# Kernel optimization log

Measured on AMD Instinct MI355X. Metric: run time of the kernel, lower is better.

## Reference

```python
import jax, jax.numpy as jnp
import numpy as np

# dims: L layers, D d_model, H heads, DH head_dim, DFF ffn, V vocab, BLK nf4 blocksize
L, D, H, DH, DFF, V, BLK = 2, 2048, 16, 128, 5504, 32000, 64
B, S, C, T = 4, 1000, 7, 45

# bitsandbytes NF4 codebook (fixed 16 quantiles of N(0,1), normalized to [-1,1])
NF4 = jnp.array([-1.0, -0.6961928009986877, -0.5250730514526367, -0.39491748809814453,
                 -0.28444138169288635, -0.18477343022823334, -0.09105003625154495, 0.0,
                 0.07958029955625534, 0.16093020141124725, 0.24611230194568634,
                 0.3379152417182922, 0.44070982933044434, 0.5626170039176941,
                 0.7229568362236023, 1.0], dtype=jnp.float32)


def _dequant(idx, scale):
    # idx: [out, in] int in [0,16); scale: [out, in//BLK] per-block absmax
    o, i = idx.shape
    return (NF4[idx].reshape(o, i // BLK, BLK) * scale[:, :, None]).reshape(o, i)


def _rmsnorm(h, w, eps=1e-5):
    return h * jax.lax.rsqrt(jnp.mean(h * h, axis=-1, keepdims=True) + eps) * w


def _rot_half(x):
    x1, x2 = jnp.split(x, 2, axis=-1)
    return jnp.concatenate([-x2, x1], axis=-1)


def _llama_fwd(token_ids, embed, wq_idx, wq_scale, wk_idx, wk_scale, wv_idx, wv_scale,
               wo_idx, wo_scale, wg_idx, wg_scale, wu_idx, wu_scale, wd_idx, wd_scale,
               ln1_w, ln2_w, lnf_w):
    Bt, St = token_ids.shape
    h = embed[token_ids]  # [B,S,D]
    # rotary embeddings
    inv = 1.0 / (10000.0 ** (jnp.arange(0, DH, 2, dtype=jnp.float32) / DH))
    ang = jnp.arange(St, dtype=jnp.float32)[:, None] * inv[None, :]  # [S, DH/2]
    emb_ang = jnp.concatenate([ang, ang], axis=-1)  # [S, DH]
    cos, sin = jnp.cos(emb_ang), jnp.sin(emb_ang)
    mask = jnp.where(jnp.tril(jnp.ones((St, St), dtype=bool)), 0.0, -1e9)  # causal
    for l in range(L):
        xn = _rmsnorm(h, ln1_w[l])
        q = (xn @ _dequant(wq_idx[l], wq_scale[l]).T).reshape(Bt, St, H, DH).transpose(0, 2, 1, 3)
        k = (xn @ _dequant(wk_idx[l], wk_scale[l]).T).reshape(Bt, St, H, DH).transpose(0, 2, 1, 3)
        v = (xn @ _dequant(wv_idx[l], wv_scale[l]).T).reshape(Bt, St, H, DH).transpose(0, 2, 1, 3)
        q = q * cos + _rot_half(q) * sin
        k = k * cos + _rot_half(k) * sin
        att = jax.nn.softmax(jnp.einsum('bhqd,bhkd->bhqk', q, k) / np.float32(np.sqrt(DH)) + mask, axis=-1)
        ctx = jnp.einsum('bhqk,bhkd->bhqd', att, v).transpose(0, 2, 1, 3).reshape(Bt, St, D)
        h = h + ctx @ _dequant(wo_idx[l], wo_scale[l]).T
        xn = _rmsnorm(h, ln2_w[l])
        g = xn @ _dequant(wg_idx[l], wg_scale[l]).T
        u = xn @ _dequant(wu_idx[l], wu_scale[l]).T
        h = h + (jax.nn.silu(g) * u) @ _dequant(wd_idx[l], wd_scale[l]).T
    # hidden_states[-1].mean(dim=1)
    return _rmsnorm(h, lnf_w).mean(axis=1)


def setup_inputs() -> dict:
    key = jax.random.key(0)
    ks = jax.random.split(key, 20)
    ridx = lambda k, shp: jax.random.randint(k, shp, 0, 16, dtype=jnp.int32)
    rsc = lambda k, shp: jax.random.uniform(k, shp, minval=0.01, maxval=0.03, dtype=jnp.float32)
    return {
        'x': jax.random.normal(ks[0], (B, C, T), dtype=jnp.float32),
        'token_ids': jax.random.randint(ks[1], (B, S), 0, V, dtype=jnp.int32),
        'embed': jax.random.normal(ks[2], (V, D), dtype=jnp.float32) * 0.02,
        'wq_idx': ridx(ks[3], (L, D, D)), 'wq_scale': rsc(ks[4], (L, D, D // BLK)),
        'wk_idx': ridx(ks[5], (L, D, D)), 'wk_scale': rsc(ks[6], (L, D, D // BLK)),
        'wv_idx': ridx(ks[7], (L, D, D)), 'wv_scale': rsc(ks[8], (L, D, D // BLK)),
        'wo_idx': ridx(ks[9], (L, D, D)), 'wo_scale': rsc(ks[10], (L, D, D // BLK)),
        'wg_idx': ridx(ks[11], (L, DFF, D)), 'wg_scale': rsc(ks[12], (L, DFF, D // BLK)),
        'wu_idx': ridx(ks[13], (L, DFF, D)), 'wu_scale': rsc(ks[14], (L, DFF, D // BLK)),
        'wd_idx': ridx(ks[15], (L, D, DFF)), 'wd_scale': rsc(ks[16], (L, D, DFF // BLK)),
        'ln1_w': jnp.ones((L, D), dtype=jnp.float32),
        'ln2_w': jnp.ones((L, D), dtype=jnp.float32),
        'lnf_w': jnp.ones((D,), dtype=jnp.float32),
        'proj_w': jax.random.normal(ks[17], (D, T), dtype=jnp.float32) * 0.05,
        'proj_b': jnp.zeros((D,), dtype=jnp.float32),
    }


def reference(x, token_ids, embed, wq_idx, wq_scale, wk_idx, wk_scale, wv_idx, wv_scale,
              wo_idx, wo_scale, wg_idx, wg_scale, wu_idx, wu_scale, wd_idx, wd_scale,
              ln1_w, ln2_w, lnf_w, proj_w, proj_b):
    # NF4-quantized Llama-style causal LM forward + mean pool over sequence
    e_text = _llama_fwd(token_ids, embed, wq_idx, wq_scale, wk_idx, wk_scale, wv_idx, wv_scale,
                        wo_idx, wo_scale, wg_idx, wg_scale, wu_idx, wu_scale, wd_idx, wd_scale,
                        ln1_w, ln2_w, lnf_w)  # [B, D]
    # series branch: channel-mean -> linear -> L2 normalize
    series_mean = x.mean(axis=1)  # [B, T]
    series_emb = series_mean @ proj_w.T + proj_b  # [B, D]
    series_emb = series_emb / jnp.maximum(jnp.linalg.norm(series_emb, axis=-1, keepdims=True), 1e-12)
    return e_text + series_emb
```

## Files before the change

kernel.cpp:

```cpp
#include <hip/hip_runtime.h>
#include <hip/hip_bf16.h>

#define L_N 2
#define D_ 2048
#define H_ 16
#define DH_ 128
#define DFF_ 5504
#define B_ 4
#define S_ 1000
#define C_ 7
#define T_ 45
#define M_ 4000

typedef short bf16x8 __attribute__((ext_vector_type(8)));
typedef float f32x4 __attribute__((ext_vector_type(4)));

__constant__ float NF4_TAB[16] = {
  -1.0f, -0.6961928009986877f, -0.5250730514526367f, -0.39491748809814453f,
  -0.28444138169288635f, -0.18477343022823334f, -0.09105003625154495f, 0.0f,
  0.07958029955625534f, 0.16093020141124725f, 0.24611230194568634f,
  0.3379152417182922f, 0.44070982933044434f, 0.5626170039176941f,
  0.7229568362236023f, 1.0f };

__device__ __forceinline__ unsigned short f2bf(float f) {
  unsigned int u = __float_as_uint(f);
  u += 0x7fffu + ((u >> 16) & 1u);
  return (unsigned short)(u >> 16);
}
__device__ __forceinline__ float bf2f(unsigned short u) {
  return __uint_as_float(((unsigned int)u) << 16);
}
__device__ __forceinline__ f32x4 zero4() { f32x4 z; z[0]=0.f; z[1]=0.f; z[2]=0.f; z[3]=0.f; return z; }
__device__ __forceinline__ f32x4 mfma16(bf16x8 a, bf16x8 b, f32x4 c) {
  return __builtin_amdgcn_mfma_f32_16x16x32_bf16(a, b, c, 0, 0, 0);
}

typedef __attribute__((address_space(3))) unsigned int lds_u32;
typedef const __attribute__((address_space(1))) unsigned int glb_u32;
__device__ __forceinline__ void gload16(const void* g, void* l) {
  __builtin_amdgcn_global_load_lds((glb_u32*)g, (lds_u32*)l, 16, 0, 0);
}

__global__ void rope_tables(float* __restrict__ cosT, float* __restrict__ sinT) {
  int s = blockIdx.x, d = threadIdx.x;
  int j = d & 63;
  float inv = expf(-(float)j * (9.210340371976184f / 64.f));
  float ang = (float)s * inv;
  cosT[s * DH_ + d] = cosf(ang);
  sinT[s * DH_ + d] = sinf(ang);
}

__global__ __launch_bounds__(256) void embed_gather(const int* __restrict__ tok,
    const float* __restrict__ emb, float* __restrict__ h) {
  int row = blockIdx.x;
  int tk = tok[row];
  const float4* src = reinterpret_cast<const float4*>(emb + (size_t)tk * D_);
  float4* dst = reinterpret_cast<float4*>(h + (size_t)row * D_);
  dst[threadIdx.x] = src[threadIdx.x];
  dst[threadIdx.x + 256] = src[threadIdx.x + 256];
}

__global__ __launch_bounds__(256) void rmsnorm_k(float* __restrict__ h,
    const float* __restrict__ add, const float* __restrict__ w,
    unsigned short* __restrict__ out) {
  const int row = blockIdx.x, t = threadIdx.x;
  float* hp = h + (size_t)row * D_;
  float4 a = *reinterpret_cast<const float4*>(&hp[t * 8]);
  float4 b = *reinterpret_cast<const float4*>(&hp[t * 8 + 4]);
  if (add) {
    const float* ap = add + (size_t)row * D_;
    float4 da = *reinterpret_cast<const float4*>(&ap[t * 8]);
    float4 db = *reinterpret_cast<const float4*>(&ap[t * 8 + 4]);
    a.x += da.x; a.y += da.y; a.z += da.z; a.w += da.w;
    b.x += db.x; b.y += db.y; b.z += db.z; b.w += db.w;
    *reinterpret_cast<float4*>(&hp[t * 8]) = a;
    *reinterpret_cast<float4*>(&hp[t * 8 + 4]) = b;
  }
  float ss = a.x*a.x + a.y*a.y + a.z*a.z + a.w*a.w
           + b.x*b.x + b.y*b.y + b.z*b.z + b.w*b.w;
#pragma unroll
  for (int m = 1; m < 64; m <<= 1) ss += __shfl_xor(ss, m);
  __shared__ float red[4];
  if ((t & 63) == 0) red[t >> 6] = ss;
  __syncthreads();
  float tot = red[0] + red[1] + red[2] + red[3];
  float rs = rsqrtf(tot * (1.0f / D_) + 1e-5f);
  float4 wa = *reinterpret_cast<const float4*>(&w[t * 8]);
  float4 wb = *reinterpret_cast<const float4*>(&w[t * 8 + 4]);
  unsigned r0 = (unsigned)f2bf(a.x*rs*wa.x) | ((unsigned)f2bf(a.y*rs*wa.y) << 16);
  unsigned r1 = (unsigned)f2bf(a.z*rs*wa.z) | ((unsigned)f2bf(a.w*rs*wa.w) << 16);
  unsigned r2 = (unsigned)f2bf(b.x*rs*wb.x) | ((unsigned)f2bf(b.y*rs*wb.y) << 16);
  unsigned r3 = (unsigned)f2bf(b.z*rs*wb.z) | ((unsigned)f2bf(b.w*rs*wb.w) << 16);
  int4 ov; ov.x = (int)r0; ov.y = (int)r1; ov.z = (int)r2; ov.w = (int)r3;
  *reinterpret_cast<int4*>(&out[(size_t)row * D_ + t * 8]) = ov;
}

struct DqJob { const int* idx; const float* sc; unsigned short* out; };
struct DqBatch { DqJob j[4]; };

__global__ __launch_bounds__(256) void dequant_batch(DqBatch bt, int K) {
  __shared__ float nf4[16];
  const int t = threadIdx.x;
  if (t < 16) nf4[t] = NF4_TAB[t];
  __syncthreads();
  const DqJob jb = bt.j[blockIdx.z];
  const int row = blockIdx.y;
  const int k0 = blockIdx.x * 2048 + t * 8;
  if (k0 >= K) return;
  const size_t base = (size_t)row * K + k0;
  int4 a = *reinterpret_cast<const int4*>(&jb.idx[base]);
  int4 b = *reinterpret_cast<const int4*>(&jb.idx[base + 4]);
  float s = jb.sc[(size_t)row * (K >> 6) + (k0 >> 6)];
  unsigned r0 = (unsigned)f2bf(nf4[a.x & 15] * s) | ((unsigned)f2bf(nf4[a.y & 15] * s) << 16);
  unsigned r1 = (unsigned)f2bf(nf4[a.z & 15] * s) | ((unsigned)f2bf(nf4[a.w & 15] * s) << 16);
  unsigned r2 = (unsigned)f2bf(nf4[b.x & 15] * s) | ((unsigned)f2bf(nf4[b.y & 15] * s) << 16);
  unsigned r3 = (unsigned)f2bf(nf4[b.z & 15] * s) | ((unsigned)f2bf(nf4[b.w & 15] * s) << 16);
  int4 ov; ov.x = (int)r0; ov.y = (int)r1; ov.z = (int)r2; ov.w = (int)r3;
  *reinterpret_cast<int4*>(&jb.out[base]) = ov;
}

template<int MODE>
__global__ __launch_bounds__(256, 4) void gemm_pipe(
    const unsigned short* __restrict__ A,
    const unsigned short* __restrict__ Bw,
    const unsigned short* __restrict__ Bw2,
    int Mdim, int N, int K,
    void* outp, void* outp2) {
  __shared__ unsigned short A_lds[2][128 * 64];
  __shared__ unsigned short B_lds[2][128 * 64];
  const int t = threadIdx.x;
  const int lane = t & 63, wid = t >> 6;
  const int z = blockIdx.z;

  const unsigned short* Bsrc = (MODE == 0 && z) ? Bw2 : Bw;
  void* osel = (MODE == 0 && z) ? outp2 : outp;

  const int bid = blockIdx.x;
  const int xcd = bid & 7, l = bid >> 3;
  const int m_blk = xcd * 4 + (l & 3);
  const int n_blk = l >> 2;
  const int n0 = n_blk * 128;
  const int m0 = m_blk * 128;

  const int wm = (wid >> 1) * 64, wn = (wid & 1) * 64;
  const int lr = lane & 15, lg = lane >> 4;
  const int lrow = lane >> 3;
  const int lslot = (((lane & 7) ^ lrow) << 4);
  const int rswz = (lr & 7) << 4;

  f32x4 acc[4][4];
#pragma unroll
  for (int i = 0; i < 4; ++i)
#pragma unroll
    for (int j = 0; j < 4; ++j) acc[i][j] = zero4();

  const int kT = K >> 6;
  const size_t rowb = (size_t)(K * 2);

  auto stage = [&](int kt, int b) {
#pragma unroll
    for (int c0 = 0; c0 < 4; ++c0) {
      const int c = wid + 4 * c0;
      int gr = m0 + c * 8 + lrow;
      gr = gr < Mdim ? gr : Mdim - 1;
      gload16((const char*)A + (size_t)gr * rowb + kt * 128 + lslot,
              (char*)&A_lds[b][0] + c * 1024);
      const int nr = n0 + c * 8 + lrow;
      gload16((const char*)Bsrc + (size_t)nr * rowb + kt * 128 + lslot,
              (char*)&B_lds[b][0] + c * 1024);
    }
  };

  stage(0, 0);
  for (int kt = 0; kt < kT; ++kt) {
    const int cur = kt & 1;
    if (kt + 1 < kT) {
      stage(kt + 1, cur ^ 1);
      asm volatile("s_waitcnt vmcnt(8)" ::: "memory");
    } else {
      asm volatile("s_waitcnt vmcnt(0)" ::: "memory");
    }
    __builtin_amdgcn_s_barrier();
    __builtin_amdgcn_sched_barrier(0);
#pragma unroll
    for (int ks = 0; ks < 2; ++ks) {
      bf16x8 af[4], bfr[4];
      const int cb = (ks * 64 + lg * 16) ^ rswz;
#pragma unroll
      for (int i = 0; i < 4; ++i) {
        af[i]  = *reinterpret_cast<const bf16x8*>(
                   (const char*)&A_lds[cur][0] + (wm + i * 16 + lr) * 128 + cb);
        bfr[i] = *reinterpret_cast<const bf16x8*>(
                   (const char*)&B_lds[cur][0] + (wn + i * 16 + lr) * 128 + cb);
      }
      __builtin_amdgcn_s_setprio(1);
#pragma unroll
      for (int mi = 0; mi < 4; ++mi)
#pragma unroll
        for (int ni = 0; ni < 4; ++ni)
          acc[mi][ni] = mfma16(af[mi], bfr[ni], acc[mi][ni]);
      __builtin_amdgcn_s_setprio(0);
    }
    __builtin_amdgcn_s_barrier();
  }

#pragma unroll
  for (int mi = 0; mi < 4; ++mi) {
#pragma unroll
    for (int r = 0; r < 4; ++r) {
      int gm = m0 + wm + mi * 16 + lg * 4 + r;
      if (gm >= Mdim) continue;
#pragma unroll
      for (int ni = 0; ni < 4; ++ni) {
        int gn = n0 + wn + ni * 16 + lr;
        float v = acc[mi][ni][r];
        if (MODE == 0) {
          ((unsigned short*)osel)[(size_t)gm * N + gn] = f2bf(v);
        } else {
          const int which = gn >> 11;
          const int hh = (gn >> 7) & 15, dd = gn & 127;
          const int b = gm / S_, s = gm - b * S_;
          ((unsigned short*)outp)[
            (((size_t)which * (B_ * H_) + b * H_ + hh) * S_ + s) * DH_ + dd] = f2bf(v);
        }
      }
    }
  }
}

template<int MODE>
__global__ __launch_bounds__(256, 4) void gemm_bf16(
    const unsigned short* __restrict__ A,
    const unsigned short* __restrict__ Bw,
    const unsigned short* __restrict__ Bw2,
    int Mdim, int N, int K, int nx, int ksplit,
    void* outp, void* outp2, float* dscr) {
  __shared__ unsigned short A_lds[128 * 64];
  __shared__ unsigned short B_lds[128 * 64];
  const int t = threadIdx.x;
  const int lane = t & 63, wid = t >> 6;
  const int z = blockIdx.z;

  const unsigned short* Bsrc = (MODE == 0 && z) ? Bw2 : Bw;
  void* osel = (MODE == 0 && z) ? outp2 : outp;

  const int bid = blockIdx.x;
  const int xcd = bid & 7, l = bid >> 3;
  const int m_blk = xcd * 4 + (l & 3);
  const int n_blk = l >> 2;
  const int n0 = n_blk * 128;
  const int m0 = m_blk * 128;

  const int wm = (wid >> 1) * 64, wn = (wid & 1) * 64;
  const int lr = lane & 15, lg = lane >> 4;
  const int lrow = lane >> 3;
  const int lslot = (((lane & 7) ^ lrow) << 4);
  const int rswz = (lr & 7) << 4;

  f32x4 acc[4][4];
#pragma unroll
  for (int i = 0; i < 4; ++i)
#pragma unroll
    for (int j = 0; j < 4; ++j) acc[i][j] = zero4();

  const int kT = K >> 6;
  const int ktlo = (MODE == 3) ? (z ? ksplit : 0) : 0;
  const int kthi = (MODE == 3) ? (z ? kT : ksplit) : kT;
  const size_t rowb = (size_t)(K * 2);

  for (int kt = ktlo; kt < kthi; ++kt) {
#pragma unroll
    for (int c0 = 0; c0 < 4; ++c0) {
      const int c = wid + 4 * c0;
      int gr = m0 + c * 8 + lrow;
      gr = gr < Mdim ? gr : Mdim - 1;
      gload16((const char*)A + (size_t)gr * rowb + kt * 128 + lslot,
              (char*)&A_lds[0] + c * 1024);
      const int nr = n0 + c * 8 + lrow;
      gload16((const char*)Bsrc + (size_t)nr * rowb + kt * 128 + lslot,
              (char*)&B_lds[0] + c * 1024);
    }
    __syncthreads();
#pragma unroll
    for (int ks = 0; ks < 2; ++ks) {
      bf16x8 af[4], bfr[4];
      const int cb = (ks * 64 + lg * 16) ^ rswz;
#pragma unroll
      for (int i = 0; i < 4; ++i) {
        af[i]  = *reinterpret_cast<const bf16x8*>(
                   (const char*)&A_lds[0] + (wm + i * 16 + lr) * 128 + cb);
        bfr[i] = *reinterpret_cast<const bf16x8*>(
                   (const char*)&B_lds[0] + (wn + i * 16 + lr) * 128 + cb);
      }
      __builtin_amdgcn_s_setprio(1);
#pragma unroll
      for (int mi = 0; mi < 4; ++mi)
#pragma unroll
        for (int ni = 0; ni < 4; ++ni)
          acc[mi][ni] = mfma16(af[mi], bfr[ni], acc[mi][ni]);
      __builtin_amdgcn_s_setprio(0);
    }
    __syncthreads();
  }

#pragma unroll
  for (int mi = 0; mi < 4; ++mi) {
#pragma unroll
    for (int r = 0; r < 4; ++r) {
      int gm = m0 + wm + mi * 16 + lg * 4 + r;
      if (gm >= Mdim) continue;
#pragma unroll
      for (int ni = 0; ni < 4; ++ni) {
        int gn = n0 + wn + ni * 16 + lr;
        float v = acc[mi][ni][r];
        if (MODE == 0) {
          ((unsigned short*)osel)[(size_t)gm * N + gn] = f2bf(v);
        } else if (MODE == 1) {
          const int which = gn >> 11;
          const int hh = (gn >> 7) & 15, dd = gn & 127;
          const int b = gm / S_, s = gm - b * S_;
          ((unsigned short*)outp)[
            (((size_t)which * (B_ * H_) + b * H_ + hh) * S_ + s) * DH_ + dd] = f2bf(v);
        } else {
          if (z == 0) ((float*)outp)[(size_t)gm * N + gn] += v;
          else        dscr[(size_t)gm * N + gn] = v;
        }
      }
    }
  }
}

__global__ __launch_bounds__(256) void silu_mul(unsigned short* __restrict__ g,
    const unsigned short* __restrict__ u) {
  const size_t i = ((size_t)blockIdx.x * 256 + threadIdx.x) * 8;
  int4 gv = *reinterpret_cast<const int4*>(&g[i]);
  int4 uv = *reinterpret_cast<const int4*>(&u[i]);
  const unsigned* gp = reinterpret_cast<const unsigned*>(&gv);
  const unsigned* up = reinterpret_cast<const unsigned*>(&uv);
  unsigned ov[4];
#pragma unroll
  for (int j = 0; j < 4; ++j) {
    float g0 = bf2f(gp[j] & 0xffffu), g1 = bf2f(gp[j] >> 16);
    float u0 = bf2f(up[j] & 0xffffu), u1 = bf2f(up[j] >> 16);
    float s0 = g0 / (1.f + __expf(-g0)) * u0;
    float s1 = g1 / (1.f + __expf(-g1)) * u1;
    ov[j] = (unsigned)f2bf(s0) | ((unsigned)f2bf(s1) << 16);
  }
  int4 o; o.x = (int)ov[0]; o.y = (int)ov[1]; o.z = (int)ov[2]; o.w = (int)ov[3];
  *reinterpret_cast<int4*>(&g[i]) = o;
}

__global__ __launch_bounds__(256) void rope_apply(unsigned short* __restrict__ qb,
    unsigned short* __restrict__ kb, const float* __restrict__ cosT,
    const float* __restrict__ sinT) {
  size_t i = (size_t)blockIdx.x * 256 + threadIdx.x;
  int d = (int)(i & 63);
  size_t row = i >> 6;
  int s = (int)(row % S_);
  size_t base = row * DH_;
  float c = cosT[s * DH_ + d], sn = sinT[s * DH_ + d];
  float q0 = bf2f(qb[base + d]), q1 = bf2f(qb[base + d + 64]);
  qb[base + d]      = f2bf(q0 * c - q1 * sn);
  qb[base + d + 64] = f2bf(q1 * c + q0 * sn);
  float k0 = bf2f(kb[base + d]), k1 = bf2f(kb[base + d + 64]);
  kb[base + d]      = f2bf(k0 * c - k1 * sn);
  kb[base + d + 64] = f2bf(k1 * c + k0 * sn);
}

__global__ __launch_bounds__(256) void vtrans_k(const unsigned short* __restrict__ vb,
    unsigned short* __restrict__ vt) {
  __shared__ unsigned int tile[64][33];
  const int t = threadIdx.x;
  const int s0 = blockIdx.x * 64, d0 = blockIdx.y * 64, bh = blockIdx.z;
#pragma unroll
  for (int j = 0; j < 2; ++j) {
    int idx = t + 256 * j;
    int s_r = idx >> 3, c8 = (idx & 7) << 3;
    int srow = s0 + s_r; srow = srow < S_ ? srow : S_ - 1;
    int4 v = *reinterpret_cast<const int4*>(&vb[((size_t)bh * S_ + srow) * DH_ + d0 + c8]);
    tile[s_r][(c8 >> 1) + 0] = (unsigned)v.x;
    tile[s_r][(c8 >> 1) + 1] = (unsigned)v.y;
    tile[s_r][(c8 >> 1) + 2] = (unsigned)v.z;
    tile[s_r][(c8 >> 1) + 3] = (unsigned)v.w;
  }
  __syncthreads();
#pragma unroll
  for (int j = 0; j < 2; ++j) {
    int idx = t + 256 * j;
    int d_r = idx >> 3, s8 = (idx & 7) << 3;
    unsigned r[8];
#pragma unroll
    for (int e = 0; e < 8; ++e) {
      unsigned wv = tile[s8 + e][d_r >> 1];
      r[e] = (d_r & 1) ? (wv >> 16) : (wv & 0xffffu);
    }
    int4 ov;
    ov.x = (int)(r[0] | (r[1] << 16));
    ov.y = (int)(r[2] | (r[3] << 16));
    ov.z = (int)(r[4] | (r[5] << 16));
    ov.w = (int)(r[6] | (r[7] << 16));
    *reinterpret_cast<int4*>(&vt[((size_t)(bh * 128 + d0 + d_r)) * 1024 + s0 + s8]) = ov;
  }
}

__global__ __launch_bounds__(512, 4) void attn2_k(const unsigned short* __restrict__ qg,
    const unsigned short* __restrict__ kg, const unsigned short* __restrict__ vtg,
    unsigned short* __restrict__ ctx) {
  __shared__ unsigned short K_lds[64 * 128];
  __shared__ unsigned short VT_lds[128 * 64];
  const int t = threadIdx.x, lane = t & 63, w = t >> 6;
  const int lr = lane & 15, lg = lane >> 4;
  const int bh = blockIdx.x, qt = blockIdx.y;
  const int q0 = qt * 128;
  const int b = bh >> 4, hh = bh & 15;
  const size_t kbase2 = (size_t)bh * S_ * DH_ * 2;
  const int q_idx = q0 + w * 16 + lr;
  const int swz = (lr & 7) << 4;

  bf16x8 qf[4];
#pragma unroll
  for (int ks = 0; ks < 4; ++ks) {
    bf16x8 z;
#pragma unroll
    for (int e = 0; e < 8; ++e) z[e] = 0;
    if (q_idx < S_)
      z = *reinterpret_cast<const bf16x8*>(
            (const char*)qg + kbase2 + (size_t)q_idx * 256 + ks * 64 + lg * 16);
    qf[ks] = z;
  }
  float mst = -1e30f, lst = 0.f;
  f32x4 cacc[8];
#pragma unroll
  for (int f = 0; f < 8; ++f) cacc[f] = zero4();

  const int q_hi = (q0 + 127 < S_) ? q0 + 127 : S_ - 1;
  const int nt = q_hi / 64 + 1;
  const int wq_max = q0 + w * 16 + 15;

  for (int kt = 0; kt < nt; ++kt) {
    const int kv0 = kt * 64;
    __syncthreads();
#pragma unroll
    for (int j = 0; j < 2; ++j) {
      const int chunk = w + 8 * j;
      int krow = chunk * 4 + (lane >> 4);
      int kcolb = (lane & 15) << 4;
      int gr = kv0 + krow; gr = gr < S_ ? gr : S_ - 1;
      gload16((const char*)kg + kbase2 + (size_t)gr * 256 + (kcolb ^ ((krow & 7) << 4)),
              (char*)K_lds + chunk * 1024);
      int vrow = chunk * 8 + (lane >> 3);
      int vcolb = (lane & 7) << 4;
      gload16((const char*)vtg + ((size_t)(bh * 128 + vrow) * 1024 + kv0) * 2 + (vcolb ^ ((vrow & 7) << 4)),
              (char*)VT_lds + chunk * 1024);
    }
    __syncthreads();
    if (kv0 > wq_max) continue;

    f32x4 sacc[4];
#pragma unroll
    for (int c = 0; c < 4; ++c) sacc[c] = zero4();
#pragma unroll
    for (int ks = 0; ks < 4; ++ks) {
#pragma unroll
      for (int c = 0; c < 4; ++c) {
        bf16x8 kf = *reinterpret_cast<const bf16x8*>(
            &K_lds[(c * 16 + lr) * 128 + (((ks * 64 + lg * 16) ^ swz) >> 1)]);
        sacc[c] = mfma16(kf, qf[ks], sacc[c]);
      }
    }
    float p[4][4];
    float mx = -1e30f;
#pragma unroll
    for (int c = 0; c < 4; ++c)
#pragma unroll
      for (int r = 0; r < 4; ++r) {
        int kv = kv0 + c * 16 + lg * 4 + r;
        float v = sacc[c][r] * 0.08838834764831845f;
        if (kv > q_idx || kv >= S_) v = -1e30f;
        p[c][r] = v;
        mx = fmaxf(mx, v);
      }
    mx = fmaxf(mx, __shfl_xor(mx, 16));
    mx = fmaxf(mx, __shfl_xor(mx, 32));
    float mn = fmaxf(mst, mx);
    float corr = __expf(mst - mn);
    mst = mn;
    float rs = 0.f;
#pragma unroll
    for (int c = 0; c < 4; ++c)
#pragma unroll
      for (int r = 0; r < 4; ++r) {
        float e = __expf(p[c][r] - mn);
        p[c][r] = e;
        rs += e;
      }
    rs += __shfl_xor(rs, 16);
    rs += __shfl_xor(rs, 32);
    lst = lst * corr + rs;
#pragma unroll
    for (int f = 0; f < 8; ++f)
#pragma unroll
      for (int r = 0; r < 4; ++r) cacc[f][r] *= corr;

    unsigned pk01[4], pk23[4];
#pragma unroll
    for (int c = 0; c < 4; ++c) {
      pk01[c] = (unsigned)f2bf(p[c][0]) | ((unsigned)f2bf(p[c][1]) << 16);
      pk23[c] = (unsigned)f2bf(p[c][2]) | ((unsigned)f2bf(p[c][3]) << 16);
    }
#pragma unroll
    for (int ks = 0; ks < 2; ++ks) {
      unsigned bu[4];
#pragma unroll
      for (int jj = 0; jj < 4; ++jj) {
        const int srcl = ((lg & 1) * 2 + (jj >> 1)) * 16 + lr;
        unsigned lo = (unsigned)__shfl((int)((jj & 1) ? pk23[2 * ks]     : pk01[2 * ks]),     srcl);
        unsigned hi = (unsigned)__shfl((int)((jj & 1) ? pk23[2 * ks + 1] : pk01[2 * ks + 1]), srcl);
        bu[jj] = (lg >= 2) ? hi : lo;
      }
      union { unsigned u[4]; bf16x8 v; } pb;
      pb.u[0] = bu[0]; pb.u[1] = bu[1]; pb.u[2] = bu[2]; pb.u[3] = bu[3];
#pragma unroll
      for (int f = 0; f < 8; ++f) {
        bf16x8 vtf = *reinterpret_cast<const bf16x8*>(
            &VT_lds[(f * 16 + lr) * 64 + (((ks * 64 + lg * 16) ^ swz) >> 1)]);
        cacc[f] = mfma16(vtf, pb.v, cacc[f]);
      }
    }
  }

  if (q_idx < S_) {
    float inv = 1.f / lst;
    unsigned short* cp = ctx + ((size_t)(b * S_ + q_idx)) * D_ + hh * 128;
#pragma unroll
    for (int f = 0; f < 8; ++f) {
      unsigned lo = (unsigned)f2bf(cacc[f][0] * inv) | ((unsigned)f2bf(cacc[f][1] * inv) << 16);
      unsigned hi = (unsigned)f2bf(cacc[f][2] * inv) | ((unsigned)f2bf(cacc[f][3] * inv) << 16);
      uint2 ov; ov.x = lo; ov.y = hi;
      *reinterpret_cast<uint2*>(cp + f * 16 + lg * 4) = ov;
    }
  }
}

__global__ __launch_bounds__(256) void meanpool(const unsigned short* __restrict__ xn,
    float* __restrict__ out) {
  int d = blockIdx.x * 256 + threadIdx.x;
  int b = blockIdx.y;
  const unsigned short* p = xn + (size_t)b * S_ * D_ + d;
  float s = 0.f;
  for (int i = 0; i < S_; ++i) s += bf2f(p[(size_t)i * D_]);
  out[(size_t)b * D_ + d] = s * (1.f / S_);
}

__global__ __launch_bounds__(256) void series_k(const float* __restrict__ x,
    const float* __restrict__ pw, const float* __restrict__ pb, float* out) {
  __shared__ float sm[T_];
  __shared__ float emb[D_];
  __shared__ float red[4];
  int b = blockIdx.x, t = threadIdx.x;
  if (t < T_) {
    float s = 0.f;
    for (int c = 0; c < C_; ++c) s += x[((size_t)b * C_ + c) * T_ + t];
    sm[t] = s * (1.f / C_);
  }
  __syncthreads();
  float ssq = 0.f;
#pragma unroll
  for (int j = 0; j < D_ / 256; ++j) {
    int d = j * 256 + t;
    float e = pb[d];
    for (int tt = 0; tt < T_; ++tt) e += sm[tt] * pw[(size_t)d * T_ + tt];
    emb[d] = e;
    ssq += e * e;
  }
#pragma unroll
  for (int m = 1; m < 64; m <<= 1) ssq += __shfl_xor(ssq, m);
  if ((t & 63) == 0) red[t >> 6] = ssq;
  __syncthreads();
  float tot = red[0] + red[1] + red[2] + red[3];
  float inv = 1.f / fmaxf(sqrtf(tot), 1e-12f);
#pragma unroll
  for (int j = 0; j < D_ / 256; ++j) {
    int d = j * 256 + t;
    out[(size_t)b * D_ + d] += emb[d] * inv;
  }
}

extern "C" void kernel_launch(void* const* d_in, const int* in_sizes, int n_in,
                              void* d_out, int out_size, void* d_ws, size_t ws_size,
                              hipStream_t stream) {
  const float* x      = (const float*)d_in[0];
  const int*   tok    = (const int*)d_in[1];
  const float* embedw = (const float*)d_in[2];
  const int*   wq_idx = (const int*)d_in[3];
  const float* wq_sc  = (const float*)d_in[4];
  const int*   wk_idx = (const int*)d_in[5];
  const float* wk_sc  = (const float*)d_in[6];
  const int*   wv_idx = (const int*)d_in[7];
  const float* wv_sc  = (const float*)d_in[8];
  const int*   wo_idx = (const int*)d_in[9];
  const float* wo_sc  = (const float*)d_in[10];
  const int*   wg_idx = (const int*)d_in[11];
  const float* wg_sc  = (const float*)d_in[12];
  const int*   wu_idx = (const int*)d_in[13];
  const float* wu_sc  = (const float*)d_in[14];
  const int*   wd_idx = (const int*)d_in[15];
  const float* wd_sc  = (const float*)d_in[16];
  const float* ln1    = (const float*)d_in[17];
  const float* ln2    = (const float*)d_in[18];
  const float* lnf    = (const float*)d_in[19];
  const float* projw  = (const float*)d_in[20];
  const float* projb  = (const float*)d_in[21];
  float* out = (float*)d_out;
  (void)in_sizes; (void)n_in; (void)out_size; (void)ws_size;

  char* wsp = (char*)d_ws;
  size_t off = 0;
  auto alloc = [&](size_t bytes) -> void* {
    void* p = wsp + off; off += (bytes + 255) & ~(size_t)255; return p; };
  float* cosT = (float*)alloc((size_t)S_ * DH_ * 4);
  float* sinT = (float*)alloc((size_t)S_ * DH_ * 4);
  float* hbuf = (float*)alloc((size_t)M_ * D_ * 4);
  unsigned short* xn   = (unsigned short*)alloc((size_t)M_ * D_ * 2);
  unsigned short* qkv  = (unsigned short*)alloc((size_t)3 * B_ * H_ * S_ * DH_ * 2);
  unsigned short* wdeq = (unsigned short*)alloc((size_t)2 * DFF_ * D_ * 2);
  unsigned short* vt   = (unsigned short*)alloc((size_t)B_ * H_ * DH_ * 1024 * 2);
  void* R = alloc((size_t)M_ * DFF_ * 2);
  float* dscr = (float*)R;
  unsigned short* ubuf = (unsigned short*)R;
  const size_t NH = (size_t)B_ * H_ * S_ * DH_;
  unsigned short* qb = qkv, *kb = qkv + NH, *vb = qkv + 2 * NH;
  unsigned short* ctx  = xn;
  unsigned short* gbuf = qkv;

  rope_tables<<<S_, DH_, 0, stream>>>(cosT, sinT);
  embed_gather<<<M_, 256, 0, stream>>>(tok, embedw, hbuf);

  const int my = (M_ + 127) / 128;
  const dim3 gQKV((3 * D_ / 128) * my);
  const dim3 gAtt((D_ / 128) * my, 1, 2);
  const dim3 gMlp((DFF_ / 128) * my, 1, 2);
  const size_t DD = (size_t)D_ * D_;
  const size_t FD = (size_t)DFF_ * D_;

  for (int l = 0; l < L_N; ++l) {
    const int*   wqi = wq_idx + (size_t)l * DD;
    const float* wqs = wq_sc + (size_t)l * D_ * (D_ / 64);
    const int*   wki = wk_idx + (size_t)l * DD;
    const float* wks = wk_sc + (size_t)l * D_ * (D_ / 64);
    const int*   wvi = wv_idx + (size_t)l * DD;
    const float* wvs = wv_sc + (size_t)l * D_ * (D_ / 64);
    const int*   woi = wo_idx + (size_t)l * DD;
    const float* wos = wo_sc + (size_t)l * D_ * (D_ / 64);
    const int*   wgi = wg_idx + (size_t)l * FD;
    const float* wgs = wg_sc + (size_t)l * DFF_ * (D_ / 64);
    const int*   wui = wu_idx + (size_t)l * FD;
    const float* wus = wu_sc + (size_t)l * DFF_ * (D_ / 64);
    const int*   wdi = wd_idx + (size_t)l * FD;
    const float* wds = wd_sc + (size_t)l * D_ * (DFF_ / 64);

    rmsnorm_k<<<M_, 256, 0, stream>>>(hbuf, l == 0 ? nullptr : dscr, ln1 + l * D_, xn);

    {
      DqBatch bt;
      bt.j[0] = { wqi, wqs, wdeq };
      bt.j[1] = { wki, wks, wdeq + DD };
      bt.j[2] = { wvi, wvs, wdeq + 2 * DD };
      bt.j[3] = { woi, wos, wdeq + 3 * DD };
      dequant_batch<<<dim3(1, D_, 4), 256, 0, stream>>>(bt, D_);
    }
    gemm_pipe<1><<<gQKV, 256, 0, stream>>>(xn, wdeq, nullptr, M_, 3 * D_, D_,
                                           qkv, nullptr);
    rope_apply<<<(B_ * H_ * S_ * 64) / 256, 256, 0, stream>>>(qb, kb, cosT, sinT);
    vtrans_k<<<dim3(16, 2, B_ * H_), 256, 0, stream>>>(vb, vt);
    attn2_k<<<dim3(B_ * H_, 8), 512, 0, stream>>>(qb, kb, vt, ctx);
    gemm_bf16<3><<<gAtt, 256, 0, stream>>>(ctx, wdeq + 3 * DD, nullptr, M_, D_, D_,
                                           D_ / 128, 16, hbuf, nullptr, dscr);
    rmsnorm_k<<<M_, 256, 0, stream>>>(hbuf, dscr, ln2 + l * D_, xn);

    {
      DqBatch bt;
      bt.j[0] = { wgi, wgs, wdeq };
      bt.j[1] = { wui, wus, wdeq + FD };
      bt.j[2] = bt.j[0]; bt.j[3] = bt.j[0];
      dequant_batch<<<dim3(1, DFF_, 2), 256, 0, stream>>>(bt, D_);
    }
    gemm_pipe<0><<<gMlp, 256, 0, stream>>>(xn, wdeq, wdeq + FD, M_, DFF_, D_,
                                           gbuf, ubuf);
    silu_mul<<<(M_ * DFF_ / 8) / 256, 256, 0, stream>>>(gbuf, ubuf);

    {
      DqBatch bt;
      bt.j[0] = { wdi, wds, wdeq };
      bt.j[1] = bt.j[0]; bt.j[2] = bt.j[0]; bt.j[3] = bt.j[0];
      dequant_batch<<<dim3(3, D_, 1), 256, 0, stream>>>(bt, DFF_);
    }
    gemm_bf16<3><<<gAtt, 256, 0, stream>>>(gbuf, wdeq, nullptr, M_, D_, DFF_,
                                           D_ / 128, 43, hbuf, nullptr, dscr);
  }

  rmsnorm_k<<<M_, 256, 0, stream>>>(hbuf, dscr, lnf, xn);
  meanpool<<<dim3(D_ / 256, B_), 256, 0, stream>>>(xn, out);
  series_k<<<B_, 256, 0, stream>>>(x, projw, projb, out);
}
```

Measured before the change: 1.425 ms.

## Fuse gate/up GEMMs with SiLU-multiply and drop double-buffered pipe GEMM

Adds a gemm_gu kernel in which each block computes the gate tile, packs it to bf16 in registers, then computes the up tile and writes silu(g)*u directly. This removes the separate silu_mul pass and the M×DFF up-projection intermediate buffer. The double-buffered gemm_pipe kernel is deleted, and the QKV projection now goes through the single-buffered gemm_bf16 path. As a result, the gate/up work runs sequentially within each block and uses half as many blocks, and the QKV GEMM loses its load/compute overlap.

```diff
diff --git a/kernel.cpp b/kernel.cpp
--- a/kernel.cpp
+++ b/kernel.cpp
@@ -120,129 +120,16 @@
 }
 
 template<int MODE>
-__global__ __launch_bounds__(256, 4) void gemm_pipe(
-    const unsigned short* __restrict__ A,
-    const unsigned short* __restrict__ Bw,
-    const unsigned short* __restrict__ Bw2,
-    int Mdim, int N, int K,
-    void* outp, void* outp2) {
-  __shared__ unsigned short A_lds[2][128 * 64];
-  __shared__ unsigned short B_lds[2][128 * 64];
-  const int t = threadIdx.x;
-  const int lane = t & 63, wid = t >> 6;
-  const int z = blockIdx.z;
-
-  const unsigned short* Bsrc = (MODE == 0 && z) ? Bw2 : Bw;
-  void* osel = (MODE == 0 && z) ? outp2 : outp;
-
-  const int bid = blockIdx.x;
-  const int xcd = bid & 7, l = bid >> 3;
-  const int m_blk = xcd * 4 + (l & 3);
-  const int n_blk = l >> 2;
-  const int n0 = n_blk * 128;
-  const int m0 = m_blk * 128;
-
-  const int wm = (wid >> 1) * 64, wn = (wid & 1) * 64;
-  const int lr = lane & 15, lg = lane >> 4;
-  const int lrow = lane >> 3;
-  const int lslot = (((lane & 7) ^ lrow) << 4);
-  const int rswz = (lr & 7) << 4;
-
-  f32x4 acc[4][4];
-#pragma unroll
-  for (int i = 0; i < 4; ++i)
-#pragma unroll
-    for (int j = 0; j < 4; ++j) acc[i][j] = zero4();
-
-  const int kT = K >> 6;
-  const size_t rowb = (size_t)(K * 2);
-
-  auto stage = [&](int kt, int b) {
-#pragma unroll
-    for (int c0 = 0; c0 < 4; ++c0) {
-      const int c = wid + 4 * c0;
-      int gr = m0 + c * 8 + lrow;
-      gr = gr < Mdim ? gr : Mdim - 1;
-      gload16((const char*)A + (size_t)gr * rowb + kt * 128 + lslot,
-              (char*)&A_lds[b][0] + c * 1024);
-      const int nr = n0 + c * 8 + lrow;
-      gload16((const char*)Bsrc + (size_t)nr * rowb + kt * 128 + lslot,
-              (char*)&B_lds[b][0] + c * 1024);
-    }
-  };
-
-  stage(0, 0);
-  for (int kt = 0; kt < kT; ++kt) {
-    const int cur = kt & 1;
-    if (kt + 1 < kT) {
-      stage(kt + 1, cur ^ 1);
-      asm volatile("s_waitcnt vmcnt(8)" ::: "memory");
-    } else {
-      asm volatile("s_waitcnt vmcnt(0)" ::: "memory");
-    }
-    __builtin_amdgcn_s_barrier();
-    __builtin_amdgcn_sched_barrier(0);
-#pragma unroll
-    for (int ks = 0; ks < 2; ++ks) {
-      bf16x8 af[4], bfr[4];
-      const int cb = (ks * 64 + lg * 16) ^ rswz;
-#pragma unroll
-      for (int i = 0; i < 4; ++i) {
-        af[i]  = *reinterpret_cast<const bf16x8*>(
-                   (const char*)&A_lds[cur][0] + (wm + i * 16 + lr) * 128 + cb);
-        bfr[i] = *reinterpret_cast<const bf16x8*>(
-                   (const char*)&B_lds[cur][0] + (wn + i * 16 + lr) * 128 + cb);
-      }
-      __builtin_amdgcn_s_setprio(1);
-#pragma unroll
-      for (int mi = 0; mi < 4; ++mi)
-#pragma unroll
-        for (int ni = 0; ni < 4; ++ni)
-          acc[mi][ni] = mfma16(af[mi], bfr[ni], acc[mi][ni]);
-      __builtin_amdgcn_s_setprio(0);
-    }
-    __builtin_amdgcn_s_barrier();
-  }
-
-#pragma unroll
-  for (int mi = 0; mi < 4; ++mi) {
-#pragma unroll
-    for (int r = 0; r < 4; ++r) {
-      int gm = m0 + wm + mi * 16 + lg * 4 + r;
-      if (gm >= Mdim) continue;
-#pragma unroll
-      for (int ni = 0; ni < 4; ++ni) {
-        int gn = n0 + wn + ni * 16 + lr;
-        float v = acc[mi][ni][r];
-        if (MODE == 0) {
-          ((unsigned short*)osel)[(size_t)gm * N + gn] = f2bf(v);
-        } else {
-          const int which = gn >> 11;
-          const int hh = (gn >> 7) & 15, dd = gn & 127;
-          const int b = gm / S_, s = gm - b * S_;
-          ((unsigned short*)outp)[
-            (((size_t)which * (B_ * H_) + b * H_ + hh) * S_ + s) * DH_ + dd] = f2bf(v);
-        }
-      }
-    }
-  }
-}
-
-template<int MODE>
 __global__ __launch_bounds__(256, 4) void gemm_bf16(
     const unsigned short* __restrict__ A,
     const unsigned short* __restrict__ Bw,
-    const unsigned short* __restrict__ Bw2,
-    int Mdim, int N, int K, int nx, int ksplit,
-    void* outp, void* outp2, float* dscr) {
+    int Mdim, int N, int K, int ksplit,
+    void* outp, float* dscr) {
   __shared__ unsigned short A_lds[128 * 64];
   __shared__ unsigned short B_lds[128 * 64];
   const int t = threadIdx.x;
   const int lane = t & 63, wid = t >> 6;
   const int z = blockIdx.z;
-
-  const unsigned short* Bsrc = (MODE == 0 && z) ? Bw2 : Bw;
-  void* osel = (MODE == 0 && z) ? outp2 : outp;
 
   const int bid = blockIdx.x;
   const int xcd = bid & 7, l = bid >> 3;
@@ -277,7 +164,7 @@
       gload16((const char*)A + (size_t)gr * rowb + kt * 128 + lslot,
               (char*)&A_lds[0] + c * 1024);
       const int nr = n0 + c * 8 + lrow;
-      gload16((const char*)Bsrc + (size_t)nr * rowb + kt * 128 + lslot,
+      gload16((const char*)Bw + (size_t)nr * rowb + kt * 128 + lslot,
               (char*)&B_lds[0] + c * 1024);
     }
     __syncthreads();
@@ -313,9 +200,7 @@
       for (int ni = 0; ni < 4; ++ni) {
         int gn = n0 + wn + ni * 16 + lr;
         float v = acc[mi][ni][r];
-        if (MODE == 0) {
-          ((unsigned short*)osel)[(size_t)gm * N + gn] = f2bf(v);
-        } else if (MODE == 1) {
+        if (MODE == 1) {
           const int which = gn >> 11;
           const int hh = (gn >> 7) & 15, dd = gn & 127;
           const int b = gm / S_, s = gm - b * S_;
@@ -330,24 +215,104 @@
   }
 }
 
-__global__ __launch_bounds__(256) void silu_mul(unsigned short* __restrict__ g,
-    const unsigned short* __restrict__ u) {
-  const size_t i = ((size_t)blockIdx.x * 256 + threadIdx.x) * 8;
-  int4 gv = *reinterpret_cast<const int4*>(&g[i]);
-  int4 uv = *reinterpret_cast<const int4*>(&u[i]);
-  const unsigned* gp = reinterpret_cast<const unsigned*>(&gv);
-  const unsigned* up = reinterpret_cast<const unsigned*>(&uv);
-  unsigned ov[4];
-#pragma unroll
-  for (int j = 0; j < 4; ++j) {
-    float g0 = bf2f(gp[j] & 0xffffu), g1 = bf2f(gp[j] >> 16);
-    float u0 = bf2f(up[j] & 0xffffu), u1 = bf2f(up[j] >> 16);
-    float s0 = g0 / (1.f + __expf(-g0)) * u0;
-    float s1 = g1 / (1.f + __expf(-g1)) * u1;
-    ov[j] = (unsigned)f2bf(s0) | ((unsigned)f2bf(s1) << 16);
-  }
-  int4 o; o.x = (int)ov[0]; o.y = (int)ov[1]; o.z = (int)ov[2]; o.w = (int)ov[3];
-  *reinterpret_cast<int4*>(&g[i]) = o;
+__global__ __launch_bounds__(256, 4) void gemm_gu(
+    const unsigned short* __restrict__ A,
+    const unsigned short* __restrict__ Bg,
+    const unsigned short* __restrict__ Bu,
+    int Mdim, int N, int K,
+    unsigned short* __restrict__ outp) {
+  __shared__ unsigned short A_lds[128 * 64];
+  __shared__ unsigned short B_lds[128 * 64];
+  const int t = threadIdx.x;
+  const int lane = t & 63, wid = t >> 6;
+
+  const int bid = blockIdx.x;
+  const int xcd = bid & 7, l = bid >> 3;
+  const int m_blk = xcd * 4 + (l & 3);
+  const int n_blk = l >> 2;
+  const int n0 = n_blk * 128;
+  const int m0 = m_blk * 128;
+
+  const int wm = (wid >> 1) * 64, wn = (wid & 1) * 64;
+  const int lr = lane & 15, lg = lane >> 4;
+  const int lrow = lane >> 3;
+  const int lslot = (((lane & 7) ^ lrow) << 4);
+  const int rswz = (lr & 7) << 4;
+
+  const int kT = K >> 6;
+  const size_t rowb = (size_t)(K * 2);
+
+  f32x4 acc[4][4];
+  unsigned pg[4][4][2];
+
+  auto kloop = [&](const unsigned short* Bsrc) {
+    for (int kt = 0; kt < kT; ++kt) {
+#pragma unroll
+      for (int c0 = 0; c0 < 4; ++c0) {
+        const int c = wid + 4 * c0;
+        int gr = m0 + c * 8 + lrow;
+        gr = gr < Mdim ? gr : Mdim - 1;
+        gload16((const char*)A + (size_t)gr * rowb + kt * 128 + lslot,
+                (char*)&A_lds[0] + c * 1024);
+        const int nr = n0 + c * 8 + lrow;
+        gload16((const char*)Bsrc + (size_t)nr * rowb + kt * 128 + lslot,
+                (char*)&B_lds[0] + c * 1024);
+      }
+      __syncthreads();
+#pragma unroll
+      for (int ks = 0; ks < 2; ++ks) {
+        bf16x8 af[4], bfr[4];
+        const int cb = (ks * 64 + lg * 16) ^ rswz;
+#pragma unroll
+        for (int i = 0; i < 4; ++i) {
+          af[i]  = *reinterpret_cast<const bf16x8*>(
+                     (const char*)&A_lds[0] + (wm + i * 16 + lr) * 128 + cb);
+          bfr[i] = *reinterpret_cast<const bf16x8*>(
+                     (const char*)&B_lds[0] + (wn + i * 16 + lr) * 128 + cb);
+        }
+        __builtin_amdgcn_s_setprio(1);
+#pragma unroll
+        for (int mi = 0; mi < 4; ++mi)
+#pragma unroll
+          for (int ni = 0; ni < 4; ++ni)
+            acc[mi][ni] = mfma16(af[mi], bfr[ni], acc[mi][ni]);
+        __builtin_amdgcn_s_setprio(0);
+      }
+      __syncthreads();
+    }
+  };
+
+#pragma unroll
+  for (int i = 0; i < 4; ++i)
+#pragma unroll
+    for (int j = 0; j < 4; ++j) acc[i][j] = zero4();
+  kloop(Bg);
+#pragma unroll
+  for (int mi = 0; mi < 4; ++mi)
+#pragma unroll
+    for (int ni = 0; ni < 4; ++ni) {
+      pg[mi][ni][0] = (unsigned)f2bf(acc[mi][ni][0]) | ((unsigned)f2bf(acc[mi][ni][1]) << 16);
+      pg[mi][ni][1] = (unsigned)f2bf(acc[mi][ni][2]) | ((unsigned)f2bf(acc[mi][ni][3]) << 16);
+      acc[mi][ni] = zero4();
+    }
+
+  kloop(Bu);
+
+#pragma unroll
+  for (int mi = 0; mi < 4; ++mi) {
+#pragma unroll
+    for (int r = 0; r < 4; ++r) {
+      int gm = m0 + wm + mi * 16 + lg * 4 + r;
+      if (gm >= Mdim) continue;
+#pragma unroll
+      for (int ni = 0; ni < 4; ++ni) {
+        int gn = n0 + wn + ni * 16 + lr;
+        float g = bf2f((unsigned short)((pg[mi][ni][r >> 1] >> ((r & 1) * 16)) & 0xffffu));
+        float sg = g / (1.f + __expf(-g));
+        outp[(size_t)gm * N + gn] = f2bf(sg * acc[mi][ni][r]);
+      }
+    }
+  }
 }
 
 __global__ __launch_bounds__(256) void rope_apply(unsigned short* __restrict__ qb,
@@ -625,9 +590,7 @@
   unsigned short* qkv  = (unsigned short*)alloc((size_t)3 * B_ * H_ * S_ * DH_ * 2);
   unsigned short* wdeq = (unsigned short*)alloc((size_t)2 * DFF_ * D_ * 2);
   unsigned short* vt   = (unsigned short*)alloc((size_t)B_ * H_ * DH_ * 1024 * 2);
-  void* R = alloc((size_t)M_ * DFF_ * 2);
-  float* dscr = (float*)R;
-  unsigned short* ubuf = (unsigned short*)R;
+  float* dscr = (float*)alloc((size_t)M_ * D_ * 4);
   const size_t NH = (size_t)B_ * H_ * S_ * DH_;
   unsigned short* qb = qkv, *kb = qkv + NH, *vb = qkv + 2 * NH;
   unsigned short* ctx  = xn;
@@ -639,7 +602,7 @@
   const int my = (M_ + 127) / 128;
   const dim3 gQKV((3 * D_ / 128) * my);
   const dim3 gAtt((D_ / 128) * my, 1, 2);
-  const dim3 gMlp((DFF_ / 128) * my, 1, 2);
+  const dim3 gGU((DFF_ / 128) * my);
   const size_t DD = (size_t)D_ * D_;
   const size_t FD = (size_t)DFF_ * D_;
 
@@ -669,13 +632,12 @@
       bt.j[3] = { woi, wos, wdeq + 3 * DD };
       dequant_batch<<<dim3(1, D_, 4), 256, 0, stream>>>(bt, D_);
     }
-    gemm_pipe<1><<<gQKV, 256, 0, stream>>>(xn, wdeq, nullptr, M_, 3 * D_, D_,
-                                           qkv, nullptr);
+    gemm_bf16<1><<<gQKV, 256, 0, stream>>>(xn, wdeq, M_, 3 * D_, D_, 0, qkv, nullptr);
     rope_apply<<<(B_ * H_ * S_ * 64) / 256, 256, 0, stream>>>(qb, kb, cosT, sinT);
     vtrans_k<<<dim3(16, 2, B_ * H_), 256, 0, stream>>>(vb, vt);
     attn2_k<<<dim3(B_ * H_, 8), 512, 0, stream>>>(qb, kb, vt, ctx);
-    gemm_bf16<3><<<gAtt, 256, 0, stream>>>(ctx, wdeq + 3 * DD, nullptr, M_, D_, D_,
-                                           D_ / 128, 16, hbuf, nullptr, dscr);
+    gemm_bf16<3><<<gAtt, 256, 0, stream>>>(ctx, wdeq + 3 * DD, M_, D_, D_, 16,
+                                           hbuf, dscr);
     rmsnorm_k<<<M_, 256, 0, stream>>>(hbuf, dscr, ln2 + l * D_, xn);
 
     {
@@ -685,9 +647,7 @@
       bt.j[2] = bt.j[0]; bt.j[3] = bt.j[0];
       dequant_batch<<<dim3(1, DFF_, 2), 256, 0, stream>>>(bt, D_);
     }
-    gemm_pipe<0><<<gMlp, 256, 0, stream>>>(xn, wdeq, wdeq + FD, M_, DFF_, D_,
-                                           gbuf, ubuf);
-    silu_mul<<<(M_ * DFF_ / 8) / 256, 256, 0, stream>>>(gbuf, ubuf);
+    gemm_gu<<<gGU, 256, 0, stream>>>(xn, wdeq, wdeq + FD, M_, DFF_, D_, gbuf);
 
     {
       DqBatch bt;
@@ -695,8 +655,8 @@
       bt.j[1] = bt.j[0]; bt.j[2] = bt.j[0]; bt.j[3] = bt.j[0];
       dequant_batch<<<dim3(3, D_, 1), 256, 0, stream>>>(bt, DFF_);
     }
-    gemm_bf16<3><<<gAtt, 256, 0, stream>>>(gbuf, wdeq, nullptr, M_, D_, DFF_,
-                                           D_ / 128, 43, hbuf, nullptr, dscr);
+    gemm_bf16<3><<<gAtt, 256, 0, stream>>>(gbuf, wdeq, M_, D_, DFF_, 43,
+                                           hbuf, dscr);
   }
 
   rmsnorm_k<<<M_, 256, 0, stream>>>(hbuf, dscr, lnf, xn);
```

Result: faster. 1.388 ms (-2.6%).
